# Optimization experiments

Measured on AMD Instinct MI355X. Metric: run time of the kernel, lower is better.

## Reference

```python
import jax, jax.numpy as jnp
import numpy as np

N = 65536      # n query/support points
NN = 34        # neighbors per point
K = 15         # kernel points
IN_F = 64
OUT_F = 64
RADIUS = 2.5
KP_EXTENT_CFG = 1.0
DENSITY = 5.0
EXTENT = KP_EXTENT_CFG * RADIUS / DENSITY  # effective KP_extent = 0.5
BN_EPS = 1e-6
LRELU_SLOPE = 0.1
POINT_DIM = 4  # modulated=True -> 3 offset dims + 1 modulation per kernel point


def make_kernel_points():
    # Deterministic stand-in for the precomputed kernel dispositions loaded
    # from disk in KPConv (fixed='center': first point at origin). Points lie
    # inside a ball of radius 1.5 * extent.
    rng = np.random.RandomState(42)
    kp = rng.normal(size=(K, 3))
    kp /= np.linalg.norm(kp, axis=1, keepdims=True)
    kp *= rng.uniform(0.3, 1.0, size=(K, 1))
    kp[0] = 0.0
    return jnp.asarray(kp * (1.5 * EXTENT), dtype=jnp.float32)


def setup_inputs() -> dict:
    key = jax.random.key(0)
    ks = jax.random.split(key, 8)
    query_points = jax.random.uniform(ks[0], (N, 3), dtype=jnp.float32)
    support_points = jax.random.uniform(ks[1], (N, 3), dtype=jnp.float32)
    neighbors_indices = jax.random.randint(ks[2], (N, NN), 0, N, dtype=jnp.int32)
    features = jax.random.normal(ks[3], (N, IN_F), dtype=jnp.float32)
    # weight_variable: truncated normal with std sqrt(2/size[-1])
    weight = jax.random.truncated_normal(ks[4], -2.0, 2.0, (K, IN_F, OUT_F), jnp.float32) * np.sqrt(2.0 / OUT_F)
    off_dim = POINT_DIM * K
    offset_weight = jax.random.truncated_normal(ks[5], -2.0, 2.0, (K, IN_F, off_dim), jnp.float32) * np.sqrt(2.0 / off_dim)
    offset_bias = jnp.zeros((off_dim,), jnp.float32)
    bn_gamma = jnp.ones((OUT_F,), jnp.float32)
    bn_beta = jnp.zeros((OUT_F,), jnp.float32)
    kernel_points = make_kernel_points()
    return dict(query_points=query_points, support_points=support_points,
                neighbors_indices=neighbors_indices, features=features,
                weight=weight, offset_weight=offset_weight, offset_bias=offset_bias,
                bn_gamma=bn_gamma, bn_beta=bn_beta, kernel_points=kernel_points)


def _influence(sq_dist):
    # KP_influence='linear': relu(1 - d / extent)
    return jax.nn.relu(1.0 - jnp.sqrt(sq_dist) / EXTENT)


def reference(query_points, support_points, neighbors_indices, features,
              weight, offset_weight, offset_bias, bn_gamma, bn_beta, kernel_points):
    n = query_points.shape[0]
    # Shadow point (far away) / shadow feature (zeros) appended at index n0
    supp_pad = jnp.concatenate([support_points, jnp.full((1, 3), 1e6, jnp.float32)], 0)
    feat_pad = jnp.concatenate([features, jnp.zeros((1, IN_F), jnp.float32)], 0)

    neigh_pts = supp_pad[neighbors_indices] - query_points[:, None, :]   # [n,nn,3]
    neigh_feats = feat_pad[neighbors_indices]                            # [n,nn,in]

    # ---- rigid KPConv producing per-point offsets (+ modulations) ----
    sq0 = jnp.sum((neigh_pts[:, :, None, :] - kernel_points[None, None]) ** 2, -1)  # [n,nn,K]
    w0 = _influence(sq0)
    wf0 = jnp.einsum('nak,nac->nkc', w0, neigh_feats)                    # [n,K,in]
    f0 = jnp.einsum('nkc,kcd->nd', wf0, offset_weight) + offset_bias     # [n,4K]
    offsets = f0[:, :3 * K].reshape(n, K, 3) * EXTENT                    # rescale to layer extent
    modulations = 2.0 * jax.nn.sigmoid(f0[:, 3 * K:])                    # [n,K]

    # ---- deformable KPConv ----
    def_kp = kernel_points[None] + offsets                               # [n,K,3]
    sq = jnp.sum((neigh_pts[:, :, None, :] - def_kp[:, None, :, :]) ** 2, -1)  # [n,nn,K]
    w = _influence(sq)                                                   # aggregation_mode='sum'
    wf = jnp.einsum('nak,nac->nkc', w, neigh_feats) * modulations[:, :, None]
    x = jnp.einsum('nkc,kco->no', wf, weight)                            # [n,out]

    # BatchNorm1d (training-mode batch stats, eps=1e-6) + LeakyReLU(0.1)
    mean = x.mean(0)
    var = x.var(0)
    x = (x - mean) * jax.lax.rsqrt(var + BN_EPS) * bn_gamma + bn_beta
    return jnp.where(x >= 0, x, LRELU_SLOPE * x)
```

## Files before the change

kernel.cpp:

```cpp
#include <hip/hip_runtime.h>
#include <math.h>

#define NPTS 65536

using half8   = __attribute__((ext_vector_type(8))) _Float16;
using half4   = __attribute__((ext_vector_type(4))) _Float16;
using floatx4 = __attribute__((ext_vector_type(4))) float;

__global__ __launch_bounds__(256) void k_prep(
    const float* __restrict__ ow, const float* __restrict__ w,
    const float* __restrict__ feat,
    _Float16* __restrict__ owt, _Float16* __restrict__ wt,
    _Float16* __restrict__ featH)
{
  int b = blockIdx.x;
  if (b < 256) {
    int i = b * 256 + threadIdx.x;
    int d = i >> 10, kc = i & 1023, c = kc >> 4, k = kc & 15;
    owt[i] = (k < 15 && d < 60) ? (_Float16)ow[(k * 64 + c) * 60 + d] : (_Float16)0.f;
    wt[i]  = (k < 15) ? (_Float16)w[(k * 64 + c) * 64 + d] : (_Float16)0.f;
  } else {
    int j = (b - 256) * 256 + threadIdx.x;
    float4 f = ((const float4*)feat)[j];
    half4 h = {(_Float16)f.x, (_Float16)f.y, (_Float16)f.z, (_Float16)f.w};
    ((half4*)featH)[j] = h;
  }
}

__global__ __launch_bounds__(256, 3) void k_fused(
    const float* __restrict__ query, const float* __restrict__ support,
    const int* __restrict__ nidx, const _Float16* __restrict__ featH,
    const float* __restrict__ kpts, const float* __restrict__ obias,
    const _Float16* __restrict__ owt, const _Float16* __restrict__ wt,
    float* __restrict__ outx)
{
  __shared__ float                  npx[16][34], npy[16][34], npz[16][34];
  __shared__ unsigned short         sidx[16][34];
  __shared__ __align__(16) _Float16 fT[4][64 * 32];
  __shared__ unsigned int           fx2[4][64];
  __shared__ __align__(16) _Float16 wfh[16 * 520];
  __shared__ float                  dk[16][64];

  const int tid  = threadIdx.x;
  const int wave = tid >> 6, lane = tid & 63;
  const int quad = lane >> 4, mm = lane & 15;
  const int base = blockIdx.x * 16;
  _Float16* fTw = fT[wave];
  unsigned int* fTw32 = (unsigned int*)fTw;
  unsigned int* fx2w = fx2[wave];
  const floatx4 fz = {0.f, 0.f, 0.f, 0.f};
  const int me = (mm < 15) ? mm : 14;

  for (int s = tid; s < 544; s += 256) {
    int pt = s / 34, a = s - pt * 34;
    int n = base + pt;
    int id = nidx[n * 34 + a];
    npx[pt][a] = support[id * 3 + 0] - query[n * 3 + 0];
    npy[pt][a] = support[id * 3 + 1] - query[n * 3 + 1];
    npz[pt][a] = support[id * 3 + 2] - query[n * 3 + 2];
    sidx[pt][a] = (unsigned short)id;
  }
  __syncthreads();

  auto load_g = [&](int pl, uint4* g0, uint4* g1) {
    #pragma unroll
    for (int it = 0; it < 3; ++it) {
      int task = it * 64 + lane;
      if (task < 136) {
        int rp = task >> 3, ch = task & 7;
        int i0 = (int)sidx[pl][2 * rp], i1 = (int)sidx[pl][2 * rp + 1];
        g0[it] = *(const uint4*)(featH + i0 * 64 + ch * 8);
        g1[it] = *(const uint4*)(featH + i1 * 64 + ch * 8);
      }
    }
  };
  auto transpose_g = [&](const uint4* g0, const uint4* g1) {
    #pragma unroll
    for (int it = 0; it < 3; ++it) {
      int task = it * 64 + lane;
      if (task < 136) {
        int rp = task >> 3, ch = task & 7;
        const uint* p0 = (const uint*)&g0[it];
        const uint* p1 = (const uint*)&g1[it];
        if (rp < 16) {
          int chunk = rp >> 2, o = rp & 3;
          #pragma unroll
          for (int cc = 0; cc < 8; ++cc) {
            int c  = ch * 8 + cc;
            int pc = chunk ^ ((ch ^ cc) & 3);
            uint v = __builtin_amdgcn_perm(p1[cc >> 1], p0[cc >> 1],
                                           (cc & 1) ? 0x07060302u : 0x05040100u);
            fTw32[c * 16 + pc * 4 + o] = v;
          }
        } else {
          #pragma unroll
          for (int cc = 0; cc < 8; ++cc) {
            uint v = __builtin_amdgcn_perm(p1[cc >> 1], p0[cc >> 1],
                                           (cc & 1) ? 0x07060302u : 0x05040100u);
            fx2w[ch * 8 + cc] = v;
          }
        }
      }
    }
  };

  auto conv_point = [&](int pl, float kx, float ky, float kz, const float* md,
                        floatx4* hold) {
    half8 a0;
    #pragma unroll
    for (int j = 0; j < 8; ++j) {
      int a = quad * 8 + j;
      float dx = npx[pl][a] - kx, dy = npy[pl][a] - ky, dz = npz[pl][a] - kz;
      float wv = 1.f - 2.f * sqrtf(dx * dx + dy * dy + dz * dz);
      a0[j] = (_Float16)fmaxf(wv, 0.f);
    }
    float w32, w33;
    {
      float dx = npx[pl][32] - kx, dy = npy[pl][32] - ky, dz = npz[pl][32] - kz;
      w32 = fmaxf(1.f - 2.f * sqrtf(dx * dx + dy * dy + dz * dz), 0.f);
      dx = npx[pl][33] - kx; dy = npy[pl][33] - ky; dz = npz[pl][33] - kz;
      w33 = fmaxf(1.f - 2.f * sqrtf(dx * dx + dy * dy + dz * dz), 0.f);
    }
    float w32r[4], w33r[4];
    #pragma unroll
    for (int r = 0; r < 4; ++r) {
      int src = (quad * 4 + r) << 2;
      w32r[r] = __int_as_float(__builtin_amdgcn_ds_bpermute(src, __float_as_int(w32)));
      w33r[r] = __int_as_float(__builtin_amdgcn_ds_bpermute(src, __float_as_int(w33)));
    }

    floatx4 acc[4];
    #pragma unroll
    for (int ct = 0; ct < 4; ++ct) {
      int c  = ct * 16 + mm;
      int pc = quad ^ (((c >> 3) ^ c) & 3);
      half8 b = *(const half8*)(fTw + c * 32 + pc * 8);
      acc[ct] = __builtin_amdgcn_mfma_f32_16x16x32_f16(a0, b, fz, 0, 0, 0);
    }
    #pragma unroll
    for (int ct = 0; ct < 4; ++ct) {
      int c = ct * 16 + mm;
      uint fp = fx2w[c];
      _Float16 lo = __builtin_bit_cast(_Float16, (unsigned short)(fp & 0xffffu));
      _Float16 hi = __builtin_bit_cast(_Float16, (unsigned short)(fp >> 16));
      float flo = (float)lo, fhi = (float)hi;
      #pragma unroll
      for (int r = 0; r < 4; ++r)
        acc[ct][r] = (acc[ct][r] + w32r[r] * flo + w33r[r] * fhi) * md[r];
    }

    _Float16* wp = wfh + pl * 520;
    #pragma unroll
    for (int ct = 0; ct < 2; ++ct) {
      half4 h = {(_Float16)acc[ct][0], (_Float16)acc[ct][1],
                 (_Float16)acc[ct][2], (_Float16)acc[ct][3]};
      *(half4*)(wp + (ct * 16 + mm) * 16 + quad * 4) = h;
    }
    hold[0] = acc[2]; hold[1] = acc[3];
  };

  auto write_hold = [&](const floatx4 (*hold)[2]) {
    #pragma unroll
    for (int pp = 0; pp < 4; ++pp) {
      _Float16* wp = wfh + (wave * 4 + pp) * 520;
      #pragma unroll
      for (int ct = 0; ct < 2; ++ct) {
        const floatx4& a = hold[pp][ct];
        half4 h = {(_Float16)a[0], (_Float16)a[1], (_Float16)a[2], (_Float16)a[3]};
        *(half4*)(wp + (ct * 16 + mm) * 16 + quad * 4) = h;
      }
    }
  };

  auto gemm_half = [&](const _Float16* bmat, int koff, floatx4& A, floatx4& B) {
    const _Float16* brow = bmat + (wave * 16 + mm) * 1024 + koff;
    const _Float16* arow = wfh + mm * 520;
    #pragma unroll
    for (int k2 = 0; k2 < 16; ++k2) {
      half8 af = *(const half8*)(arow + k2 * 32 + quad * 8);
      half8 bf = *(const half8*)(brow + k2 * 32 + quad * 8);
      if (k2 & 1) B = __builtin_amdgcn_mfma_f32_16x16x32_f16(af, bf, B, 0, 0, 0);
      else        A = __builtin_amdgcn_mfma_f32_16x16x32_f16(af, bf, A, 0, 0, 0);
    }
  };

  uint4 G0[2][3], G1[2][3];
  floatx4 hold[4][2];
  const float one4[4] = {1.f, 1.f, 1.f, 1.f};

  {
    float k0x = kpts[me * 3 + 0], k0y = kpts[me * 3 + 1], k0z = kpts[me * 3 + 2];
    load_g(wave * 4, G0[0], G1[0]);
    #pragma unroll
    for (int pp = 0; pp < 4; ++pp) {
      int pl = wave * 4 + pp;
      if (pp < 3) load_g(pl + 1, G0[(pp + 1) & 1], G1[(pp + 1) & 1]);
      transpose_g(G0[pp & 1], G1[pp & 1]);
      conv_point(pl, k0x, k0y, k0z, one4, hold[pp]);
    }
  }
  load_g(wave * 4, G0[0], G1[0]);
  __syncthreads();

  {
    floatx4 A = fz, B = fz;
    gemm_half(owt, 0, A, B);
    __syncthreads();
    write_hold(hold);
    __syncthreads();
    gemm_half(owt, 512, A, B);
    int d = wave * 16 + mm;
    float bv = (d < 60) ? obias[d] : 0.f;
    float kv = (d < 45) ? kpts[d] : 0.f;
    #pragma unroll
    for (int r = 0; r < 4; ++r) {
      int pt = quad * 4 + r;
      float v = A[r] + B[r] + bv;
      float o = (d < 45) ? (kv + 0.5f * v)
                         : (2.f / (1.f + expf(-v)));
      dk[pt][d] = o;
    }
  }
  __syncthreads();

  #pragma unroll
  for (int pp = 0; pp < 4; ++pp) {
    int pl = wave * 4 + pp;
    if (pp < 3) load_g(pl + 1, G0[(pp + 1) & 1], G1[(pp + 1) & 1]);
    float kx = dk[pl][me * 3 + 0], ky = dk[pl][me * 3 + 1], kz = dk[pl][me * 3 + 2];
    float md[4];
    #pragma unroll
    for (int r = 0; r < 4; ++r) {
      int k = quad * 4 + r;
      md[r] = (k < 15) ? dk[pl][45 + k] : 1.f;
    }
    transpose_g(G0[pp & 1], G1[pp & 1]);
    conv_point(pl, kx, ky, kz, md, hold[pp]);
  }
  __syncthreads();

  {
    floatx4 A = fz, B = fz;
    gemm_half(wt, 0, A, B);
    __syncthreads();
    write_hold(hold);
    __syncthreads();
    gemm_half(wt, 512, A, B);
    int d = wave * 16 + mm;
    #pragma unroll
    for (int r = 0; r < 4; ++r)
      outx[(base + quad * 4 + r) * 64 + d] = A[r] + B[r];
  }
}

__global__ __launch_bounds__(256) void k_stats(
    const float* __restrict__ x, float* __restrict__ stats)
{
  __shared__ float red[512];
  const int tid = threadIdx.x;
  const int c = tid & 63, g = tid >> 6;
  float s1 = 0.f, s2 = 0.f;
  for (int r = blockIdx.x * 4 + g; r < NPTS; r += 1024) {
    float v = x[r * 64 + c];
    s1 += v; s2 += v * v;
  }
  red[tid] = s1; red[256 + tid] = s2;
  __syncthreads();
  if (tid < 64) {
    s1 = red[tid] + red[tid + 64] + red[tid + 128] + red[tid + 192];
    s2 = red[256 + tid] + red[256 + tid + 64] + red[256 + tid + 128] + red[256 + tid + 192];
    atomicAdd(&stats[c], s1);
    atomicAdd(&stats[64 + c], s2);
  }
}

__global__ __launch_bounds__(256) void k_norm(
    float* __restrict__ x, const float* __restrict__ stats,
    const float* __restrict__ gamma, const float* __restrict__ beta)
{
  const int i = blockIdx.x * 256 + threadIdx.x;
  float4 v = ((float4*)x)[i];
  const int c0 = (i * 4) & 63;
  float o[4] = {v.x, v.y, v.z, v.w};
  #pragma unroll
  for (int j = 0; j < 4; ++j) {
    int c = c0 + j;
    float mean = stats[c] * (1.f / NPTS);
    float var  = stats[64 + c] * (1.f / NPTS) - mean * mean;
    float s = rsqrtf(var + 1e-6f) * gamma[c];
    float y = (o[j] - mean) * s + beta[c];
    o[j] = (y >= 0.f) ? y : 0.1f * y;
  }
  float4 rv = {o[0], o[1], o[2], o[3]};
  ((float4*)x)[i] = rv;
}

extern "C" void kernel_launch(void* const* d_in, const int* in_sizes, int n_in,
                              void* d_out, int out_size, void* d_ws, size_t ws_size,
                              hipStream_t stream)
{
  const float* query   = (const float*)d_in[0];
  const float* support = (const float*)d_in[1];
  const int*   nidx    = (const int*)d_in[2];
  const float* feat    = (const float*)d_in[3];
  const float* weight  = (const float*)d_in[4];
  const float* oweight = (const float*)d_in[5];
  const float* obias   = (const float*)d_in[6];
  const float* gamma   = (const float*)d_in[7];
  const float* beta    = (const float*)d_in[8];
  const float* kpts    = (const float*)d_in[9];
  float* x = (float*)d_out;

  char* ws = (char*)d_ws;
  _Float16* featH = (_Float16*)ws;
  _Float16* owt   = (_Float16*)(ws + 8388608);
  _Float16* wt    = (_Float16*)(ws + 8519680);
  float*    stats = (float*)(ws + 8650752);

  hipMemsetAsync(stats, 0, 512, stream);
  k_prep<<<4352, 256, 0, stream>>>(oweight, weight, feat, owt, wt, featH);
  k_fused<<<4096, 256, 0, stream>>>(query, support, nidx, featH, kpts, obias,
                                    owt, wt, x);
  k_stats<<<256, 256, 0, stream>>>(x, stats);
  k_norm<<<4096, 256, 0, stream>>>(x, stats, gamma, beta);
}
```

Baseline: 309.5 us.

## Fuse BN stats and normalize via grid barrier; restructure feature gather transpose

Merges the stats and normalize kernels into one 256-block kernel that writes per-block partial sums and waits on an atomic-counter grid barrier before normalizing its own slice. This drops the memset and one launch, and leaves each block's slice likely still cache-resident when it normalizes. The gather/transpose is reorganized so each lane loads four neighbor rows and writes uint2 pairs with a new swizzle, with the two extra neighbors stored as halves. Neighbor-position reads are vectorized as float2. The spin barrier assumes all 256 blocks are co-resident, which the hardware does not guarantee.

After: 409.9 us. +32.5%, slower.

```diff
diff --git a/kernel.cpp b/kernel.cpp
--- a/kernel.cpp
+++ b/kernel.cpp
@@ -2,6 +2,7 @@
 #include <math.h>
 
 #define NPTS 65536
+#define NBLK_SN 256
 
 using half8   = __attribute__((ext_vector_type(8))) _Float16;
 using half4   = __attribute__((ext_vector_type(4))) _Float16;
@@ -11,8 +12,9 @@
     const float* __restrict__ ow, const float* __restrict__ w,
     const float* __restrict__ feat,
     _Float16* __restrict__ owt, _Float16* __restrict__ wt,
-    _Float16* __restrict__ featH)
+    _Float16* __restrict__ featH, unsigned int* __restrict__ ctr)
 {
+  if (blockIdx.x == 0 && threadIdx.x == 0) *ctr = 0u;
   int b = blockIdx.x;
   if (b < 256) {
     int i = b * 256 + threadIdx.x;
@@ -34,20 +36,20 @@
     const _Float16* __restrict__ owt, const _Float16* __restrict__ wt,
     float* __restrict__ outx)
 {
-  __shared__ float                  npx[16][34], npy[16][34], npz[16][34];
+  __shared__ float                  np[3][16][34];
   __shared__ unsigned short         sidx[16][34];
-  __shared__ __align__(16) _Float16 fT[4][64 * 32];
-  __shared__ unsigned int           fx2[4][64];
+  __shared__ __align__(16) _Float16 fT[4][2048];
+  __shared__ __align__(16) _Float16 fxh[2][4][64];
   __shared__ __align__(16) _Float16 wfh[16 * 520];
   __shared__ float                  dk[16][64];
 
   const int tid  = threadIdx.x;
   const int wave = tid >> 6, lane = tid & 63;
   const int quad = lane >> 4, mm = lane & 15;
+  const int rq = lane >> 3, ch = lane & 7;
   const int base = blockIdx.x * 16;
   _Float16* fTw = fT[wave];
   unsigned int* fTw32 = (unsigned int*)fTw;
-  unsigned int* fx2w = fx2[wave];
   const floatx4 fz = {0.f, 0.f, 0.f, 0.f};
   const int me = (mm < 15) ? mm : 14;
 
@@ -55,72 +57,67 @@
     int pt = s / 34, a = s - pt * 34;
     int n = base + pt;
     int id = nidx[n * 34 + a];
-    npx[pt][a] = support[id * 3 + 0] - query[n * 3 + 0];
-    npy[pt][a] = support[id * 3 + 1] - query[n * 3 + 1];
-    npz[pt][a] = support[id * 3 + 2] - query[n * 3 + 2];
+    np[0][pt][a] = support[id * 3 + 0] - query[n * 3 + 0];
+    np[1][pt][a] = support[id * 3 + 1] - query[n * 3 + 1];
+    np[2][pt][a] = support[id * 3 + 2] - query[n * 3 + 2];
     sidx[pt][a] = (unsigned short)id;
   }
   __syncthreads();
 
-  auto load_g = [&](int pl, uint4* g0, uint4* g1) {
-    #pragma unroll
-    for (int it = 0; it < 3; ++it) {
-      int task = it * 64 + lane;
-      if (task < 136) {
-        int rp = task >> 3, ch = task & 7;
-        int i0 = (int)sidx[pl][2 * rp], i1 = (int)sidx[pl][2 * rp + 1];
-        g0[it] = *(const uint4*)(featH + i0 * 64 + ch * 8);
-        g1[it] = *(const uint4*)(featH + i1 * 64 + ch * 8);
-      }
-    }
-  };
-  auto transpose_g = [&](const uint4* g0, const uint4* g1) {
-    #pragma unroll
-    for (int it = 0; it < 3; ++it) {
-      int task = it * 64 + lane;
-      if (task < 136) {
-        int rp = task >> 3, ch = task & 7;
-        const uint* p0 = (const uint*)&g0[it];
-        const uint* p1 = (const uint*)&g1[it];
-        if (rp < 16) {
-          int chunk = rp >> 2, o = rp & 3;
-          #pragma unroll
-          for (int cc = 0; cc < 8; ++cc) {
-            int c  = ch * 8 + cc;
-            int pc = chunk ^ ((ch ^ cc) & 3);
-            uint v = __builtin_amdgcn_perm(p1[cc >> 1], p0[cc >> 1],
-                                           (cc & 1) ? 0x07060302u : 0x05040100u);
-            fTw32[c * 16 + pc * 4 + o] = v;
-          }
-        } else {
-          #pragma unroll
-          for (int cc = 0; cc < 8; ++cc) {
-            uint v = __builtin_amdgcn_perm(p1[cc >> 1], p0[cc >> 1],
-                                           (cc & 1) ? 0x07060302u : 0x05040100u);
-            fx2w[ch * 8 + cc] = v;
-          }
-        }
-      }
-    }
+  auto load_g = [&](int pl, uint4* G, uint4& GX) {
+    #pragma unroll
+    for (int i = 0; i < 4; ++i) {
+      int id = (int)sidx[pl][rq * 4 + i];
+      G[i] = *(const uint4*)(featH + (id << 6) + (ch << 3));
+    }
+    if (lane < 16) {
+      int id = (int)sidx[pl][32 + (lane >> 3)];
+      GX = *(const uint4*)(featH + (id << 6) + ((lane & 7) << 3));
+    }
+  };
+  auto transpose_g = [&](const uint4* G, const uint4& GX) {
+    const uint* g0 = (const uint*)&G[0];
+    const uint* g1 = (const uint*)&G[1];
+    const uint* g2 = (const uint*)&G[2];
+    const uint* g3 = (const uint*)&G[3];
+    #pragma unroll
+    for (int cc = 0; cc < 8; ++cc) {
+      int c = ch * 8 + cc;
+      uint sel = (cc & 1) ? 0x07060302u : 0x05040100u;
+      int di = cc >> 1;
+      uint2 U;
+      U.x = __builtin_amdgcn_perm(g1[di], g0[di], sel);
+      U.y = __builtin_amdgcn_perm(g3[di], g2[di], sel);
+      int rr = c ^ (ch & 1);
+      int pc = (rq >> 1) ^ ((ch ^ cc) & 3);
+      *(uint2*)(fTw32 + rr * 16 + pc * 4 + (rq & 1) * 2) = U;
+    }
+    if (lane < 16)
+      *(uint4*)(&fxh[lane >> 3][wave][(lane & 7) * 8]) = GX;
+  };
+
+  auto infl2 = [&](int pl, int pj, float kx, float ky, float kz,
+                   float& w0, float& w1) {
+    float2 px = *(const float2*)&np[0][pl][2 * pj];
+    float2 py = *(const float2*)&np[1][pl][2 * pj];
+    float2 pz = *(const float2*)&np[2][pl][2 * pj];
+    float dx = px.x - kx, dy = py.x - ky, dz = pz.x - kz;
+    w0 = fmaxf(1.f - 2.f * sqrtf(dx * dx + dy * dy + dz * dz), 0.f);
+    dx = px.y - kx; dy = py.y - ky; dz = pz.y - kz;
+    w1 = fmaxf(1.f - 2.f * sqrtf(dx * dx + dy * dy + dz * dz), 0.f);
   };
 
   auto conv_point = [&](int pl, float kx, float ky, float kz, const float* md,
                         floatx4* hold) {
     half8 a0;
     #pragma unroll
-    for (int j = 0; j < 8; ++j) {
-      int a = quad * 8 + j;
-      float dx = npx[pl][a] - kx, dy = npy[pl][a] - ky, dz = npz[pl][a] - kz;
-      float wv = 1.f - 2.f * sqrtf(dx * dx + dy * dy + dz * dz);
-      a0[j] = (_Float16)fmaxf(wv, 0.f);
+    for (int u = 0; u < 4; ++u) {
+      float w0, w1;
+      infl2(pl, quad * 4 + u, kx, ky, kz, w0, w1);
+      a0[2 * u] = (_Float16)w0; a0[2 * u + 1] = (_Float16)w1;
     }
     float w32, w33;
-    {
-      float dx = npx[pl][32] - kx, dy = npy[pl][32] - ky, dz = npz[pl][32] - kz;
-      w32 = fmaxf(1.f - 2.f * sqrtf(dx * dx + dy * dy + dz * dz), 0.f);
-      dx = npx[pl][33] - kx; dy = npy[pl][33] - ky; dz = npz[pl][33] - kz;
-      w33 = fmaxf(1.f - 2.f * sqrtf(dx * dx + dy * dy + dz * dz), 0.f);
-    }
+    infl2(pl, 16, kx, ky, kz, w32, w33);
     float w32r[4], w33r[4];
     #pragma unroll
     for (int r = 0; r < 4; ++r) {
@@ -133,17 +130,15 @@
     #pragma unroll
     for (int ct = 0; ct < 4; ++ct) {
       int c  = ct * 16 + mm;
+      int rr = c ^ ((c >> 3) & 1);
       int pc = quad ^ (((c >> 3) ^ c) & 3);
-      half8 b = *(const half8*)(fTw + c * 32 + pc * 8);
+      half8 b = *(const half8*)(fTw + rr * 32 + pc * 8);
       acc[ct] = __builtin_amdgcn_mfma_f32_16x16x32_f16(a0, b, fz, 0, 0, 0);
     }
     #pragma unroll
     for (int ct = 0; ct < 4; ++ct) {
       int c = ct * 16 + mm;
-      uint fp = fx2w[c];
-      _Float16 lo = __builtin_bit_cast(_Float16, (unsigned short)(fp & 0xffffu));
-      _Float16 hi = __builtin_bit_cast(_Float16, (unsigned short)(fp >> 16));
-      float flo = (float)lo, fhi = (float)hi;
+      float flo = (float)fxh[0][wave][c], fhi = (float)fxh[1][wave][c];
       #pragma unroll
       for (int r = 0; r < 4; ++r)
         acc[ct][r] = (acc[ct][r] + w32r[r] * flo + w33r[r] * fhi) * md[r];
@@ -184,22 +179,22 @@
     }
   };
 
-  uint4 G0[2][3], G1[2][3];
+  uint4 G[2][4], GX[2];
   floatx4 hold[4][2];
   const float one4[4] = {1.f, 1.f, 1.f, 1.f};
 
   {
     float k0x = kpts[me * 3 + 0], k0y = kpts[me * 3 + 1], k0z = kpts[me * 3 + 2];
-    load_g(wave * 4, G0[0], G1[0]);
+    load_g(wave * 4, G[0], GX[0]);
     #pragma unroll
     for (int pp = 0; pp < 4; ++pp) {
       int pl = wave * 4 + pp;
-      if (pp < 3) load_g(pl + 1, G0[(pp + 1) & 1], G1[(pp + 1) & 1]);
-      transpose_g(G0[pp & 1], G1[pp & 1]);
+      if (pp < 3) load_g(pl + 1, G[(pp + 1) & 1], GX[(pp + 1) & 1]);
+      transpose_g(G[pp & 1], GX[pp & 1]);
       conv_point(pl, k0x, k0y, k0z, one4, hold[pp]);
     }
   }
-  load_g(wave * 4, G0[0], G1[0]);
+  load_g(wave * 4, G[0], GX[0]);
   __syncthreads();
 
   {
@@ -226,7 +221,7 @@
   #pragma unroll
   for (int pp = 0; pp < 4; ++pp) {
     int pl = wave * 4 + pp;
-    if (pp < 3) load_g(pl + 1, G0[(pp + 1) & 1], G1[(pp + 1) & 1]);
+    if (pp < 3) load_g(pl + 1, G[(pp + 1) & 1], GX[(pp + 1) & 1]);
     float kx = dk[pl][me * 3 + 0], ky = dk[pl][me * 3 + 1], kz = dk[pl][me * 3 + 2];
     float md[4];
     #pragma unroll
@@ -234,7 +229,7 @@
       int k = quad * 4 + r;
       md[r] = (k < 15) ? dk[pl][45 + k] : 1.f;
     }
-    transpose_g(G0[pp & 1], G1[pp & 1]);
+    transpose_g(G[pp & 1], GX[pp & 1]);
     conv_point(pl, kx, ky, kz, md, hold[pp]);
   }
   __syncthreads();
@@ -253,46 +248,74 @@
   }
 }
 
-__global__ __launch_bounds__(256) void k_stats(
-    const float* __restrict__ x, float* __restrict__ stats)
+__global__ __launch_bounds__(256) void k_statsnorm(
+    float* __restrict__ x, float* __restrict__ part,
+    unsigned int* __restrict__ ctr,
+    const float* __restrict__ gamma, const float* __restrict__ beta)
 {
   __shared__ float red[512];
-  const int tid = threadIdx.x;
+  __shared__ float sS[64], sB[64];
+  const int tid = threadIdx.x, b = blockIdx.x;
   const int c = tid & 63, g = tid >> 6;
+
   float s1 = 0.f, s2 = 0.f;
-  for (int r = blockIdx.x * 4 + g; r < NPTS; r += 1024) {
-    float v = x[r * 64 + c];
+  const int r0 = b * 256;
+  #pragma unroll 4
+  for (int it = 0; it < 64; ++it) {
+    float v = x[(r0 + it * 4 + g) * 64 + c];
     s1 += v; s2 += v * v;
   }
   red[tid] = s1; red[256 + tid] = s2;
   __syncthreads();
-  if (tid < 64) {
-    s1 = red[tid] + red[tid + 64] + red[tid + 128] + red[tid + 192];
-    s2 = red[256 + tid] + red[256 + tid + 64] + red[256 + tid + 128] + red[256 + tid + 192];
-    atomicAdd(&stats[c], s1);
-    atomicAdd(&stats[64 + c], s2);
-  }
-}
-
-__global__ __launch_bounds__(256) void k_norm(
-    float* __restrict__ x, const float* __restrict__ stats,
-    const float* __restrict__ gamma, const float* __restrict__ beta)
-{
-  const int i = blockIdx.x * 256 + threadIdx.x;
-  float4 v = ((float4*)x)[i];
-  const int c0 = (i * 4) & 63;
-  float o[4] = {v.x, v.y, v.z, v.w};
-  #pragma unroll
-  for (int j = 0; j < 4; ++j) {
-    int c = c0 + j;
-    float mean = stats[c] * (1.f / NPTS);
-    float var  = stats[64 + c] * (1.f / NPTS) - mean * mean;
-    float s = rsqrtf(var + 1e-6f) * gamma[c];
-    float y = (o[j] - mean) * s + beta[c];
-    o[j] = (y >= 0.f) ? y : 0.1f * y;
-  }
-  float4 rv = {o[0], o[1], o[2], o[3]};
-  ((float4*)x)[i] = rv;
+  if (tid < 128) {
+    int cc = tid & 63, which = tid >> 6;
+    int o = which * 256;
+    float s = red[o + cc] + red[o + cc + 64] + red[o + cc + 128] + red[o + cc + 192];
+    part[b * 128 + which * 64 + cc] = s;
+  }
+  __threadfence();
+  __syncthreads();
+  if (tid == 0) {
+    __hip_atomic_fetch_add(ctr, 1u, __ATOMIC_RELEASE, __HIP_MEMORY_SCOPE_AGENT);
+    while (__hip_atomic_load(ctr, __ATOMIC_ACQUIRE, __HIP_MEMORY_SCOPE_AGENT)
+           < (unsigned)NBLK_SN) { __builtin_amdgcn_s_sleep(2); }
+  }
+  __syncthreads();
+
+  {
+    int c2 = tid & 127, h = tid >> 7;
+    float s = 0.f;
+    for (int bb = h * (NBLK_SN / 2); bb < (h + 1) * (NBLK_SN / 2); ++bb)
+      s += part[bb * 128 + c2];
+    red[tid] = s;
+    __syncthreads();
+    if (tid < 64) {
+      float sum = red[tid] + red[128 + tid];
+      float sq  = red[64 + tid] + red[192 + tid];
+      float mean = sum * (1.f / NPTS);
+      float var  = sq * (1.f / NPTS) - mean * mean;
+      float sc = rsqrtf(var + 1e-6f) * gamma[tid];
+      sS[tid] = sc;
+      sB[tid] = beta[tid] - mean * sc;
+    }
+    __syncthreads();
+  }
+
+  float4* x4 = (float4*)x;
+  #pragma unroll 4
+  for (int it = 0; it < 16; ++it) {
+    int i = b * 4096 + it * 256 + tid;
+    float4 v = x4[i];
+    int c0 = (i & 15) * 4;
+    float o[4] = {v.x, v.y, v.z, v.w};
+    #pragma unroll
+    for (int j = 0; j < 4; ++j) {
+      float y = o[j] * sS[c0 + j] + sB[c0 + j];
+      o[j] = (y >= 0.f) ? y : 0.1f * y;
+    }
+    float4 rv = {o[0], o[1], o[2], o[3]};
+    x4[i] = rv;
+  }
 }
 
 extern "C" void kernel_launch(void* const* d_in, const int* in_sizes, int n_in,
@@ -312,15 +335,14 @@
   float* x = (float*)d_out;
 
   char* ws = (char*)d_ws;
-  _Float16* featH = (_Float16*)ws;
-  _Float16* owt   = (_Float16*)(ws + 8388608);
-  _Float16* wt    = (_Float16*)(ws + 8519680);
-  float*    stats = (float*)(ws + 8650752);
-
-  hipMemsetAsync(stats, 0, 512, stream);
-  k_prep<<<4352, 256, 0, stream>>>(oweight, weight, feat, owt, wt, featH);
+  _Float16*     featH = (_Float16*)ws;
+  _Float16*     owt   = (_Float16*)(ws + 8388608);
+  _Float16*     wt    = (_Float16*)(ws + 8519680);
+  float*        part  = (float*)(ws + 8650752);
+  unsigned int* ctr   = (unsigned int*)(ws + 8781824);
+
+  k_prep<<<4352, 256, 0, stream>>>(oweight, weight, feat, owt, wt, featH, ctr);
   k_fused<<<4096, 256, 0, stream>>>(query, support, nidx, featH, kpts, obias,
                                     owt, wt, x);
-  k_stats<<<256, 256, 0, stream>>>(x, stats);
-  k_norm<<<4096, 256, 0, stream>>>(x, stats, gamma, beta);
+  k_statsnorm<<<NBLK_SN, 256, 0, stream>>>(x, part, ctr, gamma, beta);
 }
```
